# Kernel tuning notes

Hardware: AMD Instinct MI355X
Metric: run time of the kernel (lower is better)

Reference implementation:

```python
import jax, jax.numpy as jnp
import numpy as np

# TokenLearner 1.1 (RT-1 variant): grouped 1x1-conv MLP attention + weighted spatial mean pool.
# Grouped 1x1 convs == per-group matmuls, so we avoid materializing the g-times repeated input.

def setup_inputs() -> dict:
    key = jax.random.key(0)
    k1, k2, k3, k4, k5 = jax.random.split(key, 5)
    B, C, H, W = 32, 768, 16, 16
    G, FF = 8, 2
    D = C * FF  # inner channels per group = 1536
    x = jax.random.normal(k1, (B, C, H, W), dtype=jnp.float32)
    # conv1: groups=G, in per group = C, out per group = D
    W1 = jax.random.normal(k2, (G, D, C), dtype=jnp.float32) * (1.0 / np.sqrt(C))
    b1 = jax.random.normal(k3, (G, D), dtype=jnp.float32) * 0.02
    # conv2: groups=G, in per group = D, out per group = 1
    W2 = jax.random.normal(k4, (G, D), dtype=jnp.float32) * (1.0 / np.sqrt(D))
    b2 = jax.random.normal(k5, (G,), dtype=jnp.float32) * 0.02
    return {"x": x, "W1": W1, "b1": b1, "W2": W2, "b2": b2}


def reference(x, W1, b1, W2, b2):
    # x: [B,C,H,W]. Per-group first projection (grouped 1x1 conv on repeated x):
    # h1[b,g,d,h,w] = sum_c W1[g,d,c] * x[b,c,h,w] + b1[g,d]
    h1 = jnp.einsum('gdc,bchw->bgdhw', W1, x) + b1[None, :, :, None, None]
    h1 = jax.nn.gelu(h1, approximate=False)  # nn.GELU default is exact erf
    # second grouped 1x1 conv -> one attention logit per group
    attn = jnp.einsum('gd,bgdhw->bghw', W2, h1) + b2[None, :, None, None]
    # weighted mean pool: out[b,c,g] = mean_{h,w} x[b,c,h,w] * attn[b,g,h,w]
    Hs, Ws = x.shape[2], x.shape[3]
    out = jnp.einsum('bchw,bghw->bcg', x, attn) / (Hs * Ws)
    return out
```

## Files before the change

kernel.cpp:

```cpp
#include <hip/hip_runtime.h>
#include <hip/hip_bf16.h>
#include <cstdint>
#include <cstddef>

typedef __bf16 bf16_t;
typedef __bf16 bf16x8 __attribute__((ext_vector_type(8)));
typedef __bf16 bf16x4 __attribute__((ext_vector_type(4)));
typedef float  f32x4  __attribute__((ext_vector_type(4)));

#define AS1(p) ((const __attribute__((address_space(1))) unsigned int*)(p))
#define AS3(p) ((__attribute__((address_space(3))) unsigned int*)(p))

#if __has_builtin(__builtin_amdgcn_rcpf)
  #define FAST_RCP(x) __builtin_amdgcn_rcpf(x)
#else
  #define FAST_RCP(x) (1.0f / (x))
#endif

__device__ __forceinline__ float gelu_fast(float v) {
    float z = fabsf(v) * 0.70710678118654752440f;
    float t = FAST_RCP(fmaf(0.3275911f, z, 1.0f));
    float p = fmaf(t, 1.061405429f, -1.453152027f);
    p = fmaf(t, p, 1.421413741f);
    p = fmaf(t, p, -0.284496736f);
    p = fmaf(t, p, 0.254829592f);
    p *= t;
    float e = p * exp2f(-z * z * 1.4426950408889634f);
    float phi = (v >= 0.0f) ? fmaf(-0.5f, e, 1.0f) : (0.5f * e);
    return v * phi;
}

__global__ void k_prep(const float* __restrict__ W1, bf16_t* __restrict__ W1bf,
                       const float* __restrict__ x, bf16_t* __restrict__ xT) {
    __shared__ bf16_t t[64][66];
    int bx = blockIdx.x;
    int tid = threadIdx.x;
    if (bx < 9216) {
        int i = bx * 256 + tid;
        f32x4 v = ((const f32x4*)W1)[i];
        bf16x4 o;
        o[0] = (bf16_t)v[0]; o[1] = (bf16_t)v[1];
        o[2] = (bf16_t)v[2]; o[3] = (bf16_t)v[3];
        ((bf16x4*)W1bf)[i] = o;
        return;
    }
    int bx2 = bx - 9216;
    int ct = bx2 % 12, ht = (bx2 / 12) % 4, b = bx2 / 48;
    int col = tid & 63, rr = tid >> 6;
    const float* xb = x + ((size_t)b * 768 + (size_t)ct * 64) * 256 + ht * 64;
    #pragma unroll
    for (int r = 0; r < 16; ++r) {
        int c = r * 4 + rr;
        t[c][col] = (bf16_t)xb[(size_t)c * 256 + col];
    }
    __syncthreads();
    bf16_t* xTb = xT + ((size_t)b * 256 + (size_t)ht * 64) * 768 + ct * 64;
    #pragma unroll
    for (int r = 0; r < 16; ++r) {
        int hw = r * 4 + rr;
        xTb[(size_t)hw * 768 + col] = t[col][hw];
    }
}

__global__ __launch_bounds__(512) void k_attn_gemm(
    const bf16_t* __restrict__ W1bf, const bf16_t* __restrict__ xTbf,
    const float* __restrict__ b1, const float* __restrict__ W2,
    float* __restrict__ attn)
{
    extern __shared__ char smem[];
    bf16_t* As0 = (bf16_t*)(smem);
    bf16_t* As1 = (bf16_t*)(smem + 16384);
    bf16_t* Bs0 = (bf16_t*)(smem + 32768);
    bf16_t* Bs1 = (bf16_t*)(smem + 65536);
    float* attn_s = (float*)(smem + 98304);

    const int tid = threadIdx.x;
    const int l = tid & 63, w = tid >> 6;
    const int wm = w >> 2, wn = w & 3;
    const int bid = blockIdx.x;
    const int g     = bid & 7;
    const int local = bid >> 3;
    const int chunk = local / 24;
    const int sub   = local % 24;
    const int mt    = sub >> 1;
    const int b     = chunk * 2 + (sub & 1);

    const bf16_t* gA = W1bf + ((size_t)g * 1536 + (size_t)mt * 128) * 768;
    const bf16_t* gB = xTbf + (size_t)b * 256 * 768;

    if (tid < 256) attn_s[tid] = 0.0f;

    f32x4 acc[4][4];
    #pragma unroll
    for (int mi = 0; mi < 4; ++mi)
        #pragma unroll
        for (int ni = 0; ni < 4; ++ni)
            acc[mi][ni] = f32x4{0.0f, 0.0f, 0.0f, 0.0f};

    auto STAGE = [&](bf16_t* AsB, bf16_t* BsB, int k0) {
        #pragma unroll
        for (int i = 0; i < 2; ++i) {
            int q = i * 512 + tid;
            int row = q >> 3;
            int sc  = (q & 7) ^ (row & 7);
            __builtin_amdgcn_global_load_lds(AS1(gA + row * 768 + k0 + sc * 8),
                                             AS3((char*)AsB + q * 16), 16, 0, 0);
        }
        #pragma unroll
        for (int i = 0; i < 4; ++i) {
            int q = i * 512 + tid;
            int row = q >> 3;
            int sc  = (q & 7) ^ (row & 7);
            __builtin_amdgcn_global_load_lds(AS1(gB + row * 768 + k0 + sc * 8),
                                             AS3((char*)BsB + q * 16), 16, 0, 0);
        }
    };

    auto COMPUTE = [&](const bf16_t* AsB, const bf16_t* BsB) {
        #pragma unroll
        for (int ks = 0; ks < 2; ++ks) {
            const int c = ks * 4 + (l >> 4);
            bf16x8 af[4], bfv[4];
            #pragma unroll
            for (int mi = 0; mi < 4; ++mi) {
                int row = wm * 64 + mi * 16 + (l & 15);
                af[mi] = *(const bf16x8*)&AsB[(row * 8 + (c ^ (row & 7))) * 8];
            }
            #pragma unroll
            for (int ni = 0; ni < 4; ++ni) {
                int row = wn * 64 + ni * 16 + (l & 15);
                bfv[ni] = *(const bf16x8*)&BsB[(row * 8 + (c ^ (row & 7))) * 8];
            }
            #pragma unroll
            for (int mi = 0; mi < 4; ++mi)
                #pragma unroll
                for (int ni = 0; ni < 4; ++ni)
                    acc[mi][ni] = __builtin_amdgcn_mfma_f32_16x16x32_bf16(
                        af[mi], bfv[ni], acc[mi][ni], 0, 0, 0);
        }
    };

    STAGE(As0, Bs0, 0);
    #pragma unroll 1
    for (int kt2 = 0; kt2 < 6; ++kt2) {
        const int kt = kt2 * 2;
        STAGE(As1, Bs1, (kt + 1) * 64);
        asm volatile("s_waitcnt vmcnt(6)" ::: "memory");
        __builtin_amdgcn_s_barrier();
        COMPUTE(As0, Bs0);
        __builtin_amdgcn_s_barrier();
        if (kt + 2 < 12) {
            STAGE(As0, Bs0, (kt + 2) * 64);
            asm volatile("s_waitcnt vmcnt(6)" ::: "memory");
        } else {
            asm volatile("s_waitcnt vmcnt(0)" ::: "memory");
        }
        __builtin_amdgcn_s_barrier();
        COMPUTE(As1, Bs1);
        __builtin_amdgcn_s_barrier();
    }

    float partial[4] = {0.f, 0.f, 0.f, 0.f};
    const int r0 = (l >> 4) * 4;
    #pragma unroll
    for (int mi = 0; mi < 4; ++mi) {
        int d = mt * 128 + wm * 64 + mi * 16 + r0;
        f32x4 b1v = *(const f32x4*)&b1[g * 1536 + d];
        f32x4 w2v = *(const f32x4*)&W2[g * 1536 + d];
        #pragma unroll
        for (int j = 0; j < 4; ++j) {
            #pragma unroll
            for (int ni = 0; ni < 4; ++ni) {
                float h = acc[mi][ni][j] + b1v[j];
                partial[ni] += gelu_fast(h) * w2v[j];
            }
        }
    }
    #pragma unroll
    for (int ni = 0; ni < 4; ++ni) {
        partial[ni] += __shfl_xor(partial[ni], 16, 64);
        partial[ni] += __shfl_xor(partial[ni], 32, 64);
    }
    if (l < 16) {
        #pragma unroll
        for (int ni = 0; ni < 4; ++ni)
            atomicAdd(&attn_s[wn * 64 + ni * 16 + l], partial[ni]);
    }
    __syncthreads();
    if (tid < 256)
        atomicAdd(&attn[((size_t)b * 8 + g) * 256 + tid], attn_s[tid]);
}

__global__ void k_pool(const float* __restrict__ x, const float* __restrict__ attn,
                       const float* __restrict__ b2, float* __restrict__ out)
{
    int tid = threadIdx.x;
    int l = tid & 63, w = tid >> 6;
    int gidx = blockIdx.x * 4 + w;
    int b = gidx / 768;
    f32x4 xv = ((const f32x4*)(x + (size_t)gidx * 256))[l];
    float accg[8];
    #pragma unroll
    for (int g = 0; g < 8; ++g) {
        f32x4 av = ((const f32x4*)(attn + ((size_t)b * 8 + g) * 256))[l];
        float bb = b2[g];
        accg[g] = xv[0] * (av[0] + bb) + xv[1] * (av[1] + bb)
                + xv[2] * (av[2] + bb) + xv[3] * (av[3] + bb);
    }
    #pragma unroll
    for (int g = 0; g < 8; ++g) {
        accg[g] += __shfl_xor(accg[g], 32, 64);
        accg[g] += __shfl_xor(accg[g], 16, 64);
        accg[g] += __shfl_xor(accg[g], 8, 64);
        accg[g] += __shfl_xor(accg[g], 4, 64);
        accg[g] += __shfl_xor(accg[g], 2, 64);
        accg[g] += __shfl_xor(accg[g], 1, 64);
    }
    if (l == 0) {
        #pragma unroll
        for (int g = 0; g < 8; ++g)
            out[(size_t)gidx * 8 + g] = accg[g] * (1.0f / 256.0f);
    }
}

extern "C" void kernel_launch(void* const* d_in, const int* in_sizes, int n_in,
                              void* d_out, int out_size, void* d_ws, size_t ws_size,
                              hipStream_t stream) {
    const float* x  = (const float*)d_in[0];
    const float* W1 = (const float*)d_in[1];
    const float* b1 = (const float*)d_in[2];
    const float* W2 = (const float*)d_in[3];
    const float* b2 = (const float*)d_in[4];
    float* out = (float*)d_out;

    char* ws = (char*)d_ws;
    bf16_t* W1bf = (bf16_t*)ws;
    bf16_t* xTbf = (bf16_t*)(ws + 18874368);
    float*  attn = (float*)(ws + 18874368 + 12582912);

    hipFuncSetAttribute((const void*)k_attn_gemm,
                        hipFuncAttributeMaxDynamicSharedMemorySize, 99328);

    k_prep<<<dim3(10752), dim3(256), 0, stream>>>(W1, W1bf, x, xTbf);
    hipMemsetAsync(attn, 0, 65536 * sizeof(float), stream);
    k_attn_gemm<<<dim3(3072), dim3(512), 99328, stream>>>(W1bf, xTbf, b1, W2, attn);
    k_pool<<<dim3(6144), dim3(256), 0, stream>>>(x, attn, b2, out);
}
```

Before: 322.8 us.

## Switch GEMM to 32x32x16 MFMA with precomputed offsets and fold memset into prep

Replaces the 16x16x32 MFMA tiling with 32x32x16 bf16 MFMA, so each wave reads fewer LDS fragments per unit of compute. LDS and global offsets are precomputed once and the pipeline is peeled so the main loop has no branch. The attn zeroing moves from a separate memset into extra blocks of the prep kernel, which removes one launch. The GELU epilogue is remapped to the 32x32 accumulator layout, which risks errors in that mapping and raises register pressure.

```diff
diff --git a/kernel.cpp b/kernel.cpp
--- a/kernel.cpp
+++ b/kernel.cpp
@@ -7,6 +7,7 @@
 typedef __bf16 bf16x8 __attribute__((ext_vector_type(8)));
 typedef __bf16 bf16x4 __attribute__((ext_vector_type(4)));
 typedef float  f32x4  __attribute__((ext_vector_type(4)));
+typedef float  f32x16 __attribute__((ext_vector_type(16)));
 
 #define AS1(p) ((const __attribute__((address_space(1))) unsigned int*)(p))
 #define AS3(p) ((__attribute__((address_space(3))) unsigned int*)(p))
@@ -31,7 +32,8 @@
 }
 
 __global__ void k_prep(const float* __restrict__ W1, bf16_t* __restrict__ W1bf,
-                       const float* __restrict__ x, bf16_t* __restrict__ xT) {
+                       const float* __restrict__ x, bf16_t* __restrict__ xT,
+                       float* __restrict__ attn) {
     __shared__ bf16_t t[64][66];
     int bx = blockIdx.x;
     int tid = threadIdx.x;
@@ -44,6 +46,11 @@
         ((bf16x4*)W1bf)[i] = o;
         return;
     }
+    if (bx >= 10752) {
+        int i = (bx - 10752) * 256 + tid;
+        ((f32x4*)attn)[i] = f32x4{0.f, 0.f, 0.f, 0.f};
+        return;
+    }
     int bx2 = bx - 9216;
     int ct = bx2 % 12, ht = (bx2 / 12) % 4, b = bx2 / 48;
     int col = tid & 63, rr = tid >> 6;
@@ -68,10 +75,6 @@
     float* __restrict__ attn)
 {
     extern __shared__ char smem[];
-    bf16_t* As0 = (bf16_t*)(smem);
-    bf16_t* As1 = (bf16_t*)(smem + 16384);
-    bf16_t* Bs0 = (bf16_t*)(smem + 32768);
-    bf16_t* Bs1 = (bf16_t*)(smem + 65536);
     float* attn_s = (float*)(smem + 98304);
 
     const int tid = threadIdx.x;
@@ -85,106 +88,128 @@
     const int mt    = sub >> 1;
     const int b     = chunk * 2 + (sub & 1);
 
-    const bf16_t* gA = W1bf + ((size_t)g * 1536 + (size_t)mt * 128) * 768;
-    const bf16_t* gB = xTbf + (size_t)b * 256 * 768;
+    const bf16_t* gAk = W1bf + ((size_t)g * 1536 + (size_t)mt * 128) * 768;
+    const bf16_t* gBk = xTbf + (size_t)b * 256 * 768;
 
     if (tid < 256) attn_s[tid] = 0.0f;
 
-    f32x4 acc[4][4];
-    #pragma unroll
-    for (int mi = 0; mi < 4; ++mi)
-        #pragma unroll
-        for (int ni = 0; ni < 4; ++ni)
-            acc[mi][ni] = f32x4{0.0f, 0.0f, 0.0f, 0.0f};
-
-    auto STAGE = [&](bf16_t* AsB, bf16_t* BsB, int k0) {
-        #pragma unroll
-        for (int i = 0; i < 2; ++i) {
-            int q = i * 512 + tid;
-            int row = q >> 3;
-            int sc  = (q & 7) ^ (row & 7);
-            __builtin_amdgcn_global_load_lds(AS1(gA + row * 768 + k0 + sc * 8),
-                                             AS3((char*)AsB + q * 16), 16, 0, 0);
-        }
-        #pragma unroll
-        for (int i = 0; i < 4; ++i) {
-            int q = i * 512 + tid;
-            int row = q >> 3;
-            int sc  = (q & 7) ^ (row & 7);
-            __builtin_amdgcn_global_load_lds(AS1(gB + row * 768 + k0 + sc * 8),
-                                             AS3((char*)BsB + q * 16), 16, 0, 0);
-        }
+    int voffA[2], ldsA[2], voffB[4], ldsB[4];
+    #pragma unroll
+    for (int i = 0; i < 2; ++i) {
+        int q = i * 512 + tid, row = q >> 3, sc = (q & 7) ^ (row & 7);
+        voffA[i] = row * 768 + sc * 8;
+        ldsA[i] = q * 16;
+    }
+    #pragma unroll
+    for (int i = 0; i < 4; ++i) {
+        int q = i * 512 + tid, row = q >> 3, sc = (q & 7) ^ (row & 7);
+        voffB[i] = row * 768 + sc * 8;
+        ldsB[i] = q * 16;
+    }
+
+    const int hi = l >> 5;
+    uint32_t aoff[4][2], boff[4][2];
+    #pragma unroll
+    for (int ks = 0; ks < 4; ++ks) {
+        const int c = ks * 2 + hi;
+        #pragma unroll
+        for (int mi = 0; mi < 2; ++mi) {
+            int r = wm * 64 + mi * 32 + (l & 31);
+            aoff[ks][mi] = (uint32_t)((r * 8 + (c ^ (r & 7))) * 16);
+        }
+        #pragma unroll
+        for (int ni = 0; ni < 2; ++ni) {
+            int r = wn * 64 + ni * 32 + (l & 31);
+            boff[ks][ni] = (uint32_t)((r * 8 + (c ^ (r & 7))) * 16);
+        }
+    }
+
+    f32x16 acc[2][2];
+    #pragma unroll
+    for (int mi = 0; mi < 2; ++mi)
+        #pragma unroll
+        for (int ni = 0; ni < 2; ++ni)
+            acc[mi][ni] = (f32x16)(0.0f);
+
+    auto STAGE = [&](int abase, int bbase) {
+        #pragma unroll
+        for (int i = 0; i < 2; ++i)
+            __builtin_amdgcn_global_load_lds(AS1(gAk + voffA[i]),
+                AS3(smem + abase + ldsA[i]), 16, 0, 0);
+        #pragma unroll
+        for (int i = 0; i < 4; ++i)
+            __builtin_amdgcn_global_load_lds(AS1(gBk + voffB[i]),
+                AS3(smem + bbase + ldsB[i]), 16, 0, 0);
+        gAk += 64; gBk += 64;
     };
 
-    auto COMPUTE = [&](const bf16_t* AsB, const bf16_t* BsB) {
-        #pragma unroll
-        for (int ks = 0; ks < 2; ++ks) {
-            const int c = ks * 4 + (l >> 4);
-            bf16x8 af[4], bfv[4];
-            #pragma unroll
-            for (int mi = 0; mi < 4; ++mi) {
-                int row = wm * 64 + mi * 16 + (l & 15);
-                af[mi] = *(const bf16x8*)&AsB[(row * 8 + (c ^ (row & 7))) * 8];
+    auto COMPUTE = [&](int abase, int bbase) {
+        #pragma unroll
+        for (int ks = 0; ks < 4; ++ks) {
+            bf16x8 af[2], bfr[2];
+            #pragma unroll
+            for (int mi = 0; mi < 2; ++mi)
+                af[mi] = *(const bf16x8*)(smem + abase + aoff[ks][mi]);
+            #pragma unroll
+            for (int ni = 0; ni < 2; ++ni)
+                bfr[ni] = *(const bf16x8*)(smem + bbase + boff[ks][ni]);
+            #pragma unroll
+            for (int mi = 0; mi < 2; ++mi)
+                #pragma unroll
+                for (int ni = 0; ni < 2; ++ni)
+                    acc[mi][ni] = __builtin_amdgcn_mfma_f32_32x32x16_bf16(
+                        af[mi], bfr[ni], acc[mi][ni], 0, 0, 0);
+        }
+    };
+
+    STAGE(0, 32768);
+    #pragma unroll 1
+    for (int kt2 = 0; kt2 < 5; ++kt2) {
+        STAGE(16384, 65536);
+        asm volatile("s_waitcnt vmcnt(6)" ::: "memory");
+        __builtin_amdgcn_s_barrier();
+        COMPUTE(0, 32768);
+        __builtin_amdgcn_s_barrier();
+        STAGE(0, 32768);
+        asm volatile("s_waitcnt vmcnt(6)" ::: "memory");
+        __builtin_amdgcn_s_barrier();
+        COMPUTE(16384, 65536);
+        __builtin_amdgcn_s_barrier();
+    }
+    STAGE(16384, 65536);
+    asm volatile("s_waitcnt vmcnt(6)" ::: "memory");
+    __builtin_amdgcn_s_barrier();
+    COMPUTE(0, 32768);
+    asm volatile("s_waitcnt vmcnt(0)" ::: "memory");
+    __builtin_amdgcn_s_barrier();
+    COMPUTE(16384, 65536);
+
+    float partial[2] = {0.f, 0.f};
+    #pragma unroll
+    for (int mi = 0; mi < 2; ++mi) {
+        const int dbase = g * 1536 + mt * 128 + wm * 64 + mi * 32 + hi * 4;
+        #pragma unroll
+        for (int rq = 0; rq < 4; ++rq) {
+            f32x4 b1v = *(const f32x4*)&b1[dbase + rq * 8];
+            f32x4 w2v = *(const f32x4*)&W2[dbase + rq * 8];
+            #pragma unroll
+            for (int j = 0; j < 4; ++j) {
+                const int rg = rq * 4 + j;
+                #pragma unroll
+                for (int ni = 0; ni < 2; ++ni) {
+                    float h = acc[mi][ni][rg] + b1v[j];
+                    partial[ni] += gelu_fast(h) * w2v[j];
+                }
             }
-            #pragma unroll
-            for (int ni = 0; ni < 4; ++ni) {
-                int row = wn * 64 + ni * 16 + (l & 15);
-                bfv[ni] = *(const bf16x8*)&BsB[(row * 8 + (c ^ (row & 7))) * 8];
-            }
-            #pragma unroll
-            for (int mi = 0; mi < 4; ++mi)
-                #pragma unroll
-                for (int ni = 0; ni < 4; ++ni)
-                    acc[mi][ni] = __builtin_amdgcn_mfma_f32_16x16x32_bf16(
-                        af[mi], bfv[ni], acc[mi][ni], 0, 0, 0);
-        }
-    };
-
-    STAGE(As0, Bs0, 0);
-    #pragma unroll 1
-    for (int kt2 = 0; kt2 < 6; ++kt2) {
-        const int kt = kt2 * 2;
-        STAGE(As1, Bs1, (kt + 1) * 64);
-        asm volatile("s_waitcnt vmcnt(6)" ::: "memory");
-        __builtin_amdgcn_s_barrier();
-        COMPUTE(As0, Bs0);
-        __builtin_amdgcn_s_barrier();
-        if (kt + 2 < 12) {
-            STAGE(As0, Bs0, (kt + 2) * 64);
-            asm volatile("s_waitcnt vmcnt(6)" ::: "memory");
-        } else {
-            asm volatile("s_waitcnt vmcnt(0)" ::: "memory");
-        }
-        __builtin_amdgcn_s_barrier();
-        COMPUTE(As1, Bs1);
-        __builtin_amdgcn_s_barrier();
-    }
-
-    float partial[4] = {0.f, 0.f, 0.f, 0.f};
-    const int r0 = (l >> 4) * 4;
-    #pragma unroll
-    for (int mi = 0; mi < 4; ++mi) {
-        int d = mt * 128 + wm * 64 + mi * 16 + r0;
-        f32x4 b1v = *(const f32x4*)&b1[g * 1536 + d];
-        f32x4 w2v = *(const f32x4*)&W2[g * 1536 + d];
-        #pragma unroll
-        for (int j = 0; j < 4; ++j) {
-            #pragma unroll
-            for (int ni = 0; ni < 4; ++ni) {
-                float h = acc[mi][ni][j] + b1v[j];
-                partial[ni] += gelu_fast(h) * w2v[j];
-            }
-        }
-    }
-    #pragma unroll
-    for (int ni = 0; ni < 4; ++ni) {
-        partial[ni] += __shfl_xor(partial[ni], 16, 64);
+        }
+    }
+    #pragma unroll
+    for (int ni = 0; ni < 2; ++ni)
         partial[ni] += __shfl_xor(partial[ni], 32, 64);
-    }
-    if (l < 16) {
-        #pragma unroll
-        for (int ni = 0; ni < 4; ++ni)
-            atomicAdd(&attn_s[wn * 64 + ni * 16 + l], partial[ni]);
+    if (l < 32) {
+        #pragma unroll
+        for (int ni = 0; ni < 2; ++ni)
+            atomicAdd(&attn_s[wn * 64 + ni * 32 + l], partial[ni]);
     }
     __syncthreads();
     if (tid < 256)
@@ -241,8 +266,7 @@
     hipFuncSetAttribute((const void*)k_attn_gemm,
                         hipFuncAttributeMaxDynamicSharedMemorySize, 99328);
 
-    k_prep<<<dim3(10752), dim3(256), 0, stream>>>(W1, W1bf, x, xTbf);
-    hipMemsetAsync(attn, 0, 65536 * sizeof(float), stream);
+    k_prep<<<dim3(10816), dim3(256), 0, stream>>>(W1, W1bf, x, xTbf, attn);
     k_attn_gemm<<<dim3(3072), dim3(512), 99328, stream>>>(W1bf, xTbf, b1, W2, attn);
     k_pool<<<dim3(6144), dim3(256), 0, stream>>>(x, attn, b2, out);
 }
```

New measurement: 317.0 us. About the same (-1.8%).
